# Optimization experiments

Measured on AMD Instinct MI355X. Metric: run time of the kernel, lower is better.

The kernel has to match this reference:

```python
import jax, jax.numpy as jnp
import numpy as np

# dims: P points, CIN in_channels (z), COUT out_channels (v), T n_terms (a/b),
# N spatial index extent (i and j share it since pair_features is reused), X summed axis
P, CIN, COUT, T, N, X = 64, 16, 16, 4, 32, 64
EINSUM = 'pzijx,paix,pbjx,azv,bzv->pvij'


def setup_inputs() -> dict:
    key = jax.random.key(0)
    k0, k1, k2, k3 = jax.random.split(key, 4)
    features_weighted = jax.random.normal(k0, (P, CIN, N, N, X), dtype=jnp.float32)
    pair_features = jax.random.normal(k1, (P, T, N, X), dtype=jnp.float32)
    # kaiming_uniform fan_in (relu): bound = sqrt(6 / fan_in); emulate scale with normal init
    scale = np.float32(np.sqrt(2.0 / CIN))
    w0 = jax.random.normal(k2, (T, CIN, COUT), dtype=jnp.float32) * scale
    w1 = jax.random.normal(k3, (T, CIN, COUT), dtype=jnp.float32) * scale
    bias = jnp.zeros((COUT, 1, 1), dtype=jnp.float32)  # (out_channels,) + (1,)*(n_dim-1)
    return {
        'features_weighted': features_weighted,
        'pair_features': pair_features,
        'w0': w0,
        'w1': w1,
        'bias': bias,
    }


def reference(features_weighted, pair_features, w0, w1, bias):
    # multi-tensor contraction: pair_features enters twice (as 'paix' and 'pbjx')
    feats = jnp.einsum(EINSUM, features_weighted, pair_features, pair_features, w0, w1)
    # feats: (P, COUT, N, N); bias (COUT,1,1) broadcasts over the two spatial dims
    return jax.nn.relu(feats + bias)
```

## Files before the change

kernel.cpp:

```cpp
#include <hip/hip_runtime.h>

#define NP    64
#define NCIN  16
#define NCOUT 16
#define NT    4
#define NN    32
#define NX    64

typedef __attribute__((ext_vector_type(8))) __bf16 bf16x8;
typedef __attribute__((ext_vector_type(4))) float  f32x4;

__device__ __forceinline__ unsigned pk_bf16(float lo, float hi) {
    unsigned ulo = __float_as_uint(lo) + 0x8000u;
    unsigned uhi = __float_as_uint(hi) + 0x8000u;
    return __builtin_amdgcn_perm(uhi, ulo, 0x07060302u);
}

__global__ __launch_bounds__(256) void higher_point_kernel(
    const float* __restrict__ FW,
    const float* __restrict__ PF,
    const float* __restrict__ W0,
    const float* __restrict__ W1,
    const float* __restrict__ BIAS,
    float* __restrict__ OUT)
{
    __shared__ float pf_lds[NT * NN * NX];

    const int bx   = blockIdx.x;
    const int p    = bx >> 5;
    const int i    = bx & 31;
    const int tid  = threadIdx.x;
    const int lane = tid & 63;
    const int wave = tid >> 6;

    {
        const float4* pf_g = (const float4*)(PF + p * (NT * NN * NX));
        float4* pf_s = (float4*)pf_lds;
        #pragma unroll
        for (int k = 0; k < 8; ++k) pf_s[tid + k * 256] = pf_g[tid + k * 256];
    }
    __syncthreads();

    const int c = lane & 15;
    const int q = lane >> 4;
    const int aIdx = c >> 2;
    const int bIdx = c & 3;

    float ww[4][16];
    #pragma unroll
    for (int r = 0; r < 4; ++r) {
        const int z = q * 4 + r;
        const float4* w0r = (const float4*)(W0 + (aIdx * NCIN + z) * NCOUT);
        const float4* w1r = (const float4*)(W1 + (bIdx * NCIN + z) * NCOUT);
        #pragma unroll
        for (int t4i = 0; t4i < 4; ++t4i) {
            float4 x0 = w0r[t4i], x1 = w1r[t4i];
            ww[r][t4i * 4 + 0] = x0.x * x1.x;
            ww[r][t4i * 4 + 1] = x0.y * x1.y;
            ww[r][t4i * 4 + 2] = x0.z * x1.z;
            ww[r][t4i * 4 + 3] = x0.w * x1.w;
        }
    }

    const float biasv = BIAS[lane >> 2];

    float pfi0[8], pfi1[8];
    {
        const float* base = pf_lds + (aIdx * NN + i) * NX + q * 8;
        #pragma unroll
        for (int e = 0; e < 8; ++e) { pfi0[e] = base[e]; pfi1[e] = base[32 + e]; }
    }

    const float* fw_row = FW + ((p * NCIN + c) * (NN * NN) + i * NN) * NX + q * 8;

    const int j0 = wave * 8;

    float4 nf0a, nf0b, nf1a, nf1b;
    {
        const float* rb = fw_row + j0 * NX;
        nf0a = ((const float4*)rb)[0];
        nf0b = ((const float4*)rb)[1];
        nf1a = ((const float4*)(rb + 32))[0];
        nf1b = ((const float4*)(rb + 32))[1];
    }

    for (int jj = 0; jj < 8; ++jj) {
        const int j = j0 + jj;
        float4 f0a = nf0a, f0b = nf0b, f1a = nf1a, f1b = nf1b;
        if (jj < 7) {
            const float* rb = fw_row + (j + 1) * NX;
            nf0a = ((const float4*)rb)[0];
            nf0b = ((const float4*)rb)[1];
            nf1a = ((const float4*)(rb + 32))[0];
            nf1b = ((const float4*)(rb + 32))[1];
        }

        float pfj0[8], pfj1[8];
        {
            const float* base = pf_lds + (bIdx * NN + j) * NX + q * 8;
            #pragma unroll
            for (int e = 0; e < 8; ++e) { pfj0[e] = base[e]; pfj1[e] = base[32 + e]; }
        }

        union { unsigned u[4]; bf16x8 v; } A0, A1, B0, B1;
        A0.u[0] = pk_bf16(f0a.x, f0a.y); A0.u[1] = pk_bf16(f0a.z, f0a.w);
        A0.u[2] = pk_bf16(f0b.x, f0b.y); A0.u[3] = pk_bf16(f0b.z, f0b.w);
        A1.u[0] = pk_bf16(f1a.x, f1a.y); A1.u[1] = pk_bf16(f1a.z, f1a.w);
        A1.u[2] = pk_bf16(f1b.x, f1b.y); A1.u[3] = pk_bf16(f1b.z, f1b.w);

        float r0[8], r1[8];
        #pragma unroll
        for (int e = 0; e < 8; ++e) { r0[e] = pfi0[e] * pfj0[e]; r1[e] = pfi1[e] * pfj1[e]; }
        B0.u[0] = pk_bf16(r0[0], r0[1]); B0.u[1] = pk_bf16(r0[2], r0[3]);
        B0.u[2] = pk_bf16(r0[4], r0[5]); B0.u[3] = pk_bf16(r0[6], r0[7]);
        B1.u[0] = pk_bf16(r1[0], r1[1]); B1.u[1] = pk_bf16(r1[2], r1[3]);
        B1.u[2] = pk_bf16(r1[4], r1[5]); B1.u[3] = pk_bf16(r1[6], r1[7]);

        f32x4 acc = {0.f, 0.f, 0.f, 0.f};
        acc = __builtin_amdgcn_mfma_f32_16x16x32_bf16(A0.v, B0.v, acc, 0, 0, 0);
        acc = __builtin_amdgcn_mfma_f32_16x16x32_bf16(A1.v, B1.v, acc, 0, 0, 0);

        float partial[16];
        #pragma unroll
        for (int v = 0; v < 16; ++v)
            partial[v] = acc[0] * ww[0][v] + acc[1] * ww[1][v]
                       + acc[2] * ww[2][v] + acc[3] * ww[3][v];

        const bool b5 = (lane & 32) != 0;
        const bool b4 = (lane & 16) != 0;
        const bool b3 = (lane & 8)  != 0;
        const bool b2 = (lane & 4)  != 0;

        float t8[8];
        #pragma unroll
        for (int k = 0; k < 8; ++k) {
            float mine   = b5 ? partial[k + 8] : partial[k];
            float theirs = b5 ? partial[k]     : partial[k + 8];
            t8[k] = mine + __shfl_xor(theirs, 32, 64);
        }
        float t4[4];
        #pragma unroll
        for (int k = 0; k < 4; ++k) {
            float mine   = b4 ? t8[k + 4] : t8[k];
            float theirs = b4 ? t8[k]     : t8[k + 4];
            t4[k] = mine + __shfl_xor(theirs, 16, 64);
        }
        float t2[2];
        #pragma unroll
        for (int k = 0; k < 2; ++k) {
            float mine   = b3 ? t4[k + 2] : t4[k];
            float theirs = b3 ? t4[k]     : t4[k + 2];
            t2[k] = mine + __shfl_xor(theirs, 8, 64);
        }
        float mine1   = b2 ? t2[1] : t2[0];
        float theirs1 = b2 ? t2[0] : t2[1];
        float s = mine1 + __shfl_xor(theirs1, 4, 64);
        s += __shfl_xor(s, 2, 64);
        s += __shfl_xor(s, 1, 64);

        if ((lane & 3) == 0) {
            float rv = s + biasv;
            OUT[((p * NCOUT + (lane >> 2)) * NN + i) * NN + j] = rv > 0.f ? rv : 0.f;
        }
    }
}

extern "C" void kernel_launch(void* const* d_in, const int* in_sizes, int n_in,
                              void* d_out, int out_size, void* d_ws, size_t ws_size,
                              hipStream_t stream) {
    const float* FW   = (const float*)d_in[0];
    const float* PF   = (const float*)d_in[1];
    const float* W0   = (const float*)d_in[2];
    const float* W1   = (const float*)d_in[3];
    const float* BIAS = (const float*)d_in[4];
    float* OUT = (float*)d_out;

    hipLaunchKernelGGL(higher_point_kernel, dim3(NP * NN), dim3(256), 0, stream,
                       FW, PF, W0, W1, BIAS, OUT);
}
```

Before: 371.3 us.

## Replace scalar weight contraction and shuffle reduction with a second MFMA stage

The (a,b,z)->v weight contraction and the cross-lane shuffle reduction are replaced by a second bf16 MFMA stage. Each j's first-stage accumulator is split into hi and lo bf16 parts to keep precision and stored into swizzled LDS. Pairwise weight products are precomputed into LDS as bf16, and each wave then does a 16x16x256 MFMA before writing bias+ReLU output. The aim is to remove the heavy per-j FMA and shuffle work. In exchange it adds LDS traffic (about 48KB per block plus an extra barrier), which may limit occupancy, and it rounds the weights to bf16.

```diff
diff --git a/kernel.cpp b/kernel.cpp
--- a/kernel.cpp
+++ b/kernel.cpp
@@ -16,7 +16,7 @@
     return __builtin_amdgcn_perm(uhi, ulo, 0x07060302u);
 }
 
-__global__ __launch_bounds__(256) void higher_point_kernel(
+__global__ __launch_bounds__(256, 2) void higher_point_kernel(
     const float* __restrict__ FW,
     const float* __restrict__ PF,
     const float* __restrict__ W0,
@@ -24,7 +24,9 @@
     const float* __restrict__ BIAS,
     float* __restrict__ OUT)
 {
-    __shared__ float pf_lds[NT * NN * NX];
+    __shared__ __align__(16) float pf_lds[NT * NN * NX];
+    __shared__ __align__(16) unsigned short ww_lds[16 * 256];
+    __shared__ __align__(16) unsigned short q_lds[4][8 * 512];
 
     const int bx   = blockIdx.x;
     const int p    = bx >> 5;
@@ -39,30 +41,29 @@
         #pragma unroll
         for (int k = 0; k < 8; ++k) pf_s[tid + k * 256] = pf_g[tid + k * 256];
     }
+
+    {
+        const int v  = tid >> 4;
+        const int ab = tid & 15;
+        const int a  = ab >> 2, b = ab & 3;
+        float prod[16];
+        #pragma unroll
+        for (int z = 0; z < 16; ++z)
+            prod[z] = W0[(a * NCIN + z) * NCOUT + v] * W1[(b * NCIN + z) * NCOUT + v];
+        unsigned pw[8];
+        #pragma unroll
+        for (int t = 0; t < 8; ++t) pw[t] = pk_bf16(prod[2 * t], prod[2 * t + 1]);
+        char* base = (char*)ww_lds + v * 512;
+        const int swz = (v & 7) << 4;
+        *(uint4*)(base + ((ab * 32) ^ swz))      = make_uint4(pw[0], pw[1], pw[2], pw[3]);
+        *(uint4*)(base + ((ab * 32 + 16) ^ swz)) = make_uint4(pw[4], pw[5], pw[6], pw[7]);
+    }
     __syncthreads();
 
     const int c = lane & 15;
     const int q = lane >> 4;
     const int aIdx = c >> 2;
     const int bIdx = c & 3;
-
-    float ww[4][16];
-    #pragma unroll
-    for (int r = 0; r < 4; ++r) {
-        const int z = q * 4 + r;
-        const float4* w0r = (const float4*)(W0 + (aIdx * NCIN + z) * NCOUT);
-        const float4* w1r = (const float4*)(W1 + (bIdx * NCIN + z) * NCOUT);
-        #pragma unroll
-        for (int t4i = 0; t4i < 4; ++t4i) {
-            float4 x0 = w0r[t4i], x1 = w1r[t4i];
-            ww[r][t4i * 4 + 0] = x0.x * x1.x;
-            ww[r][t4i * 4 + 1] = x0.y * x1.y;
-            ww[r][t4i * 4 + 2] = x0.z * x1.z;
-            ww[r][t4i * 4 + 3] = x0.w * x1.w;
-        }
-    }
-
-    const float biasv = BIAS[lane >> 2];
 
     float pfi0[8], pfi1[8];
     {
@@ -120,47 +121,57 @@
         acc = __builtin_amdgcn_mfma_f32_16x16x32_bf16(A0.v, B0.v, acc, 0, 0, 0);
         acc = __builtin_amdgcn_mfma_f32_16x16x32_bf16(A1.v, B1.v, acc, 0, 0, 0);
 
-        float partial[16];
+        unsigned ua0 = __float_as_uint(acc[0]) + 0x8000u;
+        unsigned ua1 = __float_as_uint(acc[1]) + 0x8000u;
+        unsigned ua2 = __float_as_uint(acc[2]) + 0x8000u;
+        unsigned ua3 = __float_as_uint(acc[3]) + 0x8000u;
+        unsigned qhi01 = __builtin_amdgcn_perm(ua1, ua0, 0x07060302u);
+        unsigned qhi23 = __builtin_amdgcn_perm(ua3, ua2, 0x07060302u);
+        float l0 = acc[0] - __uint_as_float(ua0 & 0xffff0000u);
+        float l1 = acc[1] - __uint_as_float(ua1 & 0xffff0000u);
+        float l2 = acc[2] - __uint_as_float(ua2 & 0xffff0000u);
+        float l3 = acc[3] - __uint_as_float(ua3 & 0xffff0000u);
+        unsigned qlo01 = pk_bf16(l0, l1);
+        unsigned qlo23 = pk_bf16(l2, l3);
+
+        char* qrow = (char*)q_lds[wave] + jj * 1024 + ((c * 32 + q * 8) ^ (jj << 4));
+        *(uint2*)(qrow)       = make_uint2(qhi01, qhi23);
+        *(uint2*)(qrow + 512) = make_uint2(qlo01, qlo23);
+    }
+    __syncthreads();
+
+    const int swzc = (c & 7) << 4;
+    const char* wwbase = (const char*)ww_lds + c * 512;
+    const char* qbase  = (const char*)q_lds[wave] + (c & 7) * 1024;
+    const int qoff = q * 16;
+
+    uint4 aw[8];
+    #pragma unroll
+    for (int m = 0; m < 8; ++m)
+        aw[m] = *(const uint4*)(wwbase + ((m * 64 + qoff) ^ swzc));
+
+    f32x4 acc2 = {0.f, 0.f, 0.f, 0.f};
+    #pragma unroll
+    for (int pl = 0; pl < 2; ++pl) {
         #pragma unroll
-        for (int v = 0; v < 16; ++v)
-            partial[v] = acc[0] * ww[0][v] + acc[1] * ww[1][v]
-                       + acc[2] * ww[2][v] + acc[3] * ww[3][v];
+        for (int m = 0; m < 8; ++m) {
+            union { uint4 u; bf16x8 v; } av, qb;
+            av.u = aw[m];
+            qb.u = *(const uint4*)(qbase + pl * 512 + ((m * 64 + qoff) ^ swzc));
+            acc2 = __builtin_amdgcn_mfma_f32_16x16x32_bf16(av.v, qb.v, acc2, 0, 0, 0);
+        }
+    }
 
-        const bool b5 = (lane & 32) != 0;
-        const bool b4 = (lane & 16) != 0;
-        const bool b3 = (lane & 8)  != 0;
-        const bool b2 = (lane & 4)  != 0;
-
-        float t8[8];
+    if (c < 8) {
+        const int j = j0 + c;
+        const float4 b4 = *(const float4*)(BIAS + q * 4);
+        float bb[4] = {b4.x, b4.y, b4.z, b4.w};
+        float* op = OUT + (p * NCOUT * NN + i) * NN + j;
         #pragma unroll
-        for (int k = 0; k < 8; ++k) {
-            float mine   = b5 ? partial[k + 8] : partial[k];
-            float theirs = b5 ? partial[k]     : partial[k + 8];
-            t8[k] = mine + __shfl_xor(theirs, 32, 64);
-        }
-        float t4[4];
-        #pragma unroll
-        for (int k = 0; k < 4; ++k) {
-            float mine   = b4 ? t8[k + 4] : t8[k];
-            float theirs = b4 ? t8[k]     : t8[k + 4];
-            t4[k] = mine + __shfl_xor(theirs, 16, 64);
-        }
-        float t2[2];
-        #pragma unroll
-        for (int k = 0; k < 2; ++k) {
-            float mine   = b3 ? t4[k + 2] : t4[k];
-            float theirs = b3 ? t4[k]     : t4[k + 2];
-            t2[k] = mine + __shfl_xor(theirs, 8, 64);
-        }
-        float mine1   = b2 ? t2[1] : t2[0];
-        float theirs1 = b2 ? t2[0] : t2[1];
-        float s = mine1 + __shfl_xor(theirs1, 4, 64);
-        s += __shfl_xor(s, 2, 64);
-        s += __shfl_xor(s, 1, 64);
-
-        if ((lane & 3) == 0) {
-            float rv = s + biasv;
-            OUT[((p * NCOUT + (lane >> 2)) * NN + i) * NN + j] = rv > 0.f ? rv : 0.f;
+        for (int r = 0; r < 4; ++r) {
+            float rv = acc2[r] + bb[r];
+            rv = rv > 0.f ? rv : 0.f;
+            op[(q * 4 + r) * (NN * NN)] = rv;
         }
     }
 }
```

New measurement: 364.0 us. About the same (-2.0%).
